# Optimization experiments

Measured on AMD Instinct MI355X. Metric: run time of the kernel, lower is better.

The kernel has to match this reference:

```python
import jax, jax.numpy as jnp
import numpy as np
from jax import lax

FT = 48   # feature map size (hardcoded as 48*48 in the torch decode)
C = 24    # backbone output channels
HC = 96   # head_conv
HEADS = {"hm_hp": 17, "hm": 1, "hps": 34, "hp_offset": 34}
DELTA = 1.8
SCALE = 0.02083333395421505  # ~1/48, exact literal from the module


def setup_inputs() -> dict:
    key = jax.random.key(0)
    ks = iter(jax.random.split(key, 64))
    inp = {"x": jax.random.normal(next(ks), (1, C, FT, FT), dtype=jnp.float32)}
    for h, cls in HEADS.items():
        inp[h + "_dw_w"] = jax.random.normal(next(ks), (C, 1, 3, 3), jnp.float32) * 0.1
        inp[h + "_dw_b"] = jax.random.normal(next(ks), (C,), jnp.float32) * 0.01
        inp[h + "_pw1_w"] = jax.random.normal(next(ks), (HC, C, 1, 1), jnp.float32) * 0.1
        inp[h + "_pw1_b"] = jax.random.normal(next(ks), (HC,), jnp.float32) * 0.01
        inp[h + "_pw2_w"] = jax.random.normal(next(ks), (cls, HC, 1, 1), jnp.float32) * 0.1
        inp[h + "_pw2_b"] = jax.random.normal(next(ks), (cls,), jnp.float32) * 0.01
    return inp


def _conv(x, w, groups=1):
    pad = "SAME" if w.shape[-1] == 3 else "VALID"
    return lax.conv_general_dilated(x, w, (1, 1), pad, feature_group_count=groups,
                                    dimension_numbers=("NCHW", "OIHW", "NCHW"))


def _head(x, dw_w, dw_b, pw1_w, pw1_b, pw2_w, pw2_b):
    y = _conv(x, dw_w, groups=C) + dw_b[None, :, None, None]
    y = jax.nn.relu(_conv(y, pw1_w) + pw1_b[None, :, None, None])
    return _conv(y, pw2_w) + pw2_b[None, :, None, None]


def _decode(hm_hp, hm, hps, hp_off):
    # NCHW [1,c,48,48] -> HWC
    kpt_heatmap = jax.nn.sigmoid(jnp.transpose(hm_hp[0], (1, 2, 0)))            # [48,48,17]
    center = jax.nn.sigmoid(jnp.transpose(hm[0], (1, 2, 0)))[:, :, 0]           # [48,48]
    kpt_regress = jnp.transpose(hps[0], (1, 2, 0)).reshape(FT * FT, 17, 2)
    kpt_offset = jnp.transpose(hp_off[0], (1, 2, 0)).reshape(FT * FT, 17, 2)

    rng = jnp.arange(FT, dtype=jnp.float32)
    gy = rng[:, None] - FT / 2.0
    gx = rng[None, :] - FT / 2.0
    w2c = 1.0 / (jnp.sqrt(gy * gy + gx * gx) + DELTA)                            # [48,48]

    # center-weighted argmax -> single center index
    ct = jnp.argmax((center * w2c).reshape(-1))
    ct_y = (ct // FT).astype(jnp.float32)
    ct_x = (ct % FT).astype(jnp.float32)

    kpt_coor = kpt_regress[ct] + jnp.stack([ct_y, ct_x])                         # [17,2]

    # distance-weighted per-keypoint argmax over the heatmap
    dy = rng[:, None, None] - kpt_coor[:, 0]                                     # [48,1,17]
    dx = rng[None, :, None] - kpt_coor[:, 1]                                     # [1,48,17]
    dist_weight = jnp.sqrt(dy * dy + dx * dx) + DELTA                            # [48,48,17]
    scores = (kpt_heatmap / dist_weight).reshape(FT * FT, 17)
    top = jnp.argmax(scores, axis=0)                                             # [17]

    ys = (top // FT).astype(jnp.float32)
    xs = (top % FT).astype(jnp.float32)
    k17 = jnp.arange(17)
    conf = kpt_heatmap.reshape(FT * FT, 17)[top, k17]                            # [17]
    off_yx = kpt_offset[top, k17]                                                # [17,2]
    coord = (off_yx + jnp.stack([ys, xs], axis=1)) * SCALE                       # [17,2]
    return jnp.concatenate([coord, conf[:, None]], axis=1).reshape(1, 1, 17, 3)


def _forward(x,
             hm_hp_dw_w, hm_hp_dw_b, hm_hp_pw1_w, hm_hp_pw1_b, hm_hp_pw2_w, hm_hp_pw2_b,
             hm_dw_w, hm_dw_b, hm_pw1_w, hm_pw1_b, hm_pw2_w, hm_pw2_b,
             hps_dw_w, hps_dw_b, hps_pw1_w, hps_pw1_b, hps_pw2_w, hps_pw2_b,
             hp_offset_dw_w, hp_offset_dw_b, hp_offset_pw1_w, hp_offset_pw1_b, hp_offset_pw2_w, hp_offset_pw2_b):
    x = x * 0.007843137718737125 - 1.0  # module's input normalization (backbone = identity)
    hm_hp = _head(x, hm_hp_dw_w, hm_hp_dw_b, hm_hp_pw1_w, hm_hp_pw1_b, hm_hp_pw2_w, hm_hp_pw2_b)
    hm = _head(x, hm_dw_w, hm_dw_b, hm_pw1_w, hm_pw1_b, hm_pw2_w, hm_pw2_b)
    hps = _head(x, hps_dw_w, hps_dw_b, hps_pw1_w, hps_pw1_b, hps_pw2_w, hps_pw2_b)
    hp_off = _head(x, hp_offset_dw_w, hp_offset_dw_b, hp_offset_pw1_w, hp_offset_pw1_b, hp_offset_pw2_w, hp_offset_pw2_b)
    return _decode(hm_hp, hm, hps, hp_off)


def reference(x,
              hm_hp_dw_w, hm_hp_dw_b, hm_hp_pw1_w, hm_hp_pw1_b, hm_hp_pw2_w, hm_hp_pw2_b,
              hm_dw_w, hm_dw_b, hm_pw1_w, hm_pw1_b, hm_pw2_w, hm_pw2_b,
              hps_dw_w, hps_dw_b, hps_pw1_w, hps_pw1_b, hps_pw2_w, hps_pw2_b,
              hp_offset_dw_w, hp_offset_dw_b, hp_offset_pw1_w, hp_offset_pw1_b, hp_offset_pw2_w, hp_offset_pw2_b):
    return _forward(x,
                    hm_hp_dw_w, hm_hp_dw_b, hm_hp_pw1_w, hm_hp_pw1_b, hm_hp_pw2_w, hm_hp_pw2_b,
                    hm_dw_w, hm_dw_b, hm_pw1_w, hm_pw1_b, hm_pw2_w, hm_pw2_b,
                    hps_dw_w, hps_dw_b, hps_pw1_w, hps_pw1_b, hps_pw2_w, hps_pw2_b,
                    hp_offset_dw_w, hp_offset_dw_b, hp_offset_pw1_w, hp_offset_pw1_b, hp_offset_pw2_w, hp_offset_pw2_b)
```

## Files before the change

kernel.cpp:

```cpp
#include <hip/hip_runtime.h>
#include <math.h>

#define FT 48
#define NPIX 2304
#define CIN 24
#define HC 96
#define NORM_SCALE 0.007843137718737125f
#define OUT_SCALE 0.02083333395421505f
#define DELTA 1.8f
#define NPROD 144
#define NDEC 17

__device__ int g_counter = 0;
__device__ int g_done = 0;

struct PF {
    const float* x;
    const float* w[4][6];
    float* hmhp_sig;
    float* pval;
    int*   pidx;
    float* out;
};

__device__ __forceinline__ float sigmoidf_(float v) { return 1.0f / (1.0f + expf(-v)); }

__global__ __launch_bounds__(256) void fused(PF p)
{
    __shared__ float s_dww[216];
    __shared__ float s_dwb[24];
    __shared__ float s_pw1w[HC * CIN];
    __shared__ float s_pw1b[HC];
    __shared__ float s_pw2t[HC * 17];
    __shared__ float s_pw2b[17];
    __shared__ float sv[4];
    __shared__ int si[4];
    __shared__ int s_ticket;
    __shared__ float s2_dww[2][216];
    __shared__ float s2_dwb[2][24];
    __shared__ float s2_pw1[2][HC * CIN];
    __shared__ float s2_pw1b[2][HC];
    __shared__ float s2_pw2[2][2 * HC];
    __shared__ float s2_pw2b[2][2];
    __shared__ float s_red[256];
    __shared__ int s_redi[256];
    __shared__ float s_dwv[CIN];
    __shared__ float sA[HC];
    __shared__ float s_ky, s_kx;
    __shared__ int s_ct, s_top;

    const int t = threadIdx.x;
    const int b = blockIdx.x;
    const bool is_hm = (b >= 72);
    const int lb = is_hm ? b - 72 : b;
    const int head = is_hm ? 1 : 0;

    const float* dw_w  = p.w[head][0];
    const float* dw_b  = p.w[head][1];
    const float* pw1_w = p.w[head][2];
    const float* pw1_b = p.w[head][3];
    const float* pw2_w = p.w[head][4];
    const float* pw2_b = p.w[head][5];

    if (t < 216) s_dww[t] = dw_w[t];
    if (t < 24) s_dwb[t] = dw_b[t];
    for (int i = t; i < HC * CIN; i += 256) s_pw1w[i] = pw1_w[i];
    if (t < HC) s_pw1b[t] = pw1_b[t];
    if (!is_hm) {
        for (int i = t; i < HC * 17; i += 256) {
            const int co = i / 17, k = i - co * 17;
            s_pw2t[i] = pw2_w[k * HC + co];
        }
        if (t < 17) s_pw2b[t] = pw2_b[t];
    } else {
        if (t < HC) s_pw2t[t] = pw2_w[t];
        if (t == 0) s_pw2b[0] = pw2_b[0];
    }

    const int lane = t & 63;
    const int split = lane & 7;
    const int pix = lb * 32 + (t >> 3);
    const int py = pix / FT;
    const int px = pix % FT;

    float xt[3][9];
#pragma unroll
    for (int c = 0; c < 3; ++c) {
        const int ci = split * 3 + c;
#pragma unroll
        for (int ky = 0; ky < 3; ++ky) {
            const int yy = py + ky - 1;
#pragma unroll
            for (int kx = 0; kx < 3; ++kx) {
                const int xx = px + kx - 1;
                float v = 0.0f;
                if (yy >= 0 && yy < FT && xx >= 0 && xx < FT)
                    v = p.x[ci * NPIX + yy * FT + xx] * NORM_SCALE - 1.0f;
                xt[c][ky * 3 + kx] = v;
            }
        }
    }
    __syncthreads();

    float part[3];
#pragma unroll
    for (int c = 0; c < 3; ++c) {
        const int ci = split * 3 + c;
        float acc = s_dwb[ci];
#pragma unroll
        for (int tap = 0; tap < 9; ++tap)
            acc = fmaf(s_dww[ci * 9 + tap], xt[c][tap], acc);
        part[c] = acc;
    }

    float dwv[CIN];
    const int gbase = lane & ~7;
#pragma unroll
    for (int ci = 0; ci < CIN; ++ci) {
        const float v = (ci % 3 == 0) ? part[0] : ((ci % 3 == 1) ? part[1] : part[2]);
        dwv[ci] = __shfl(v, gbase | (ci / 3), 64);
    }

    if (!is_hm) {
        float oacc[17];
#pragma unroll
        for (int k = 0; k < 17; ++k) oacc[k] = 0.0f;
#pragma unroll 4
        for (int j = 0; j < 12; ++j) {
            const int co = j * 8 + split;
            float a = s_pw1b[co];
#pragma unroll
            for (int ci = 0; ci < CIN; ++ci)
                a = fmaf(s_pw1w[co * CIN + ci], dwv[ci], a);
            a = fmaxf(a, 0.0f);
#pragma unroll
            for (int k = 0; k < 17; ++k)
                oacc[k] = fmaf(s_pw2t[co * 17 + k], a, oacc[k]);
        }
#pragma unroll
        for (int off = 1; off < 8; off <<= 1)
#pragma unroll
            for (int k = 0; k < 17; ++k)
                oacc[k] += __shfl_xor(oacc[k], off, 64);
        {
            int k = split;
            p.hmhp_sig[k * NPIX + pix] = sigmoidf_(oacc[k] + s_pw2b[k]);
            k = split + 8;
            p.hmhp_sig[k * NPIX + pix] = sigmoidf_(oacc[k] + s_pw2b[k]);
            if (split == 0)
                p.hmhp_sig[16 * NPIX + pix] = sigmoidf_(oacc[16] + s_pw2b[16]);
        }
    } else {
        float acc1 = 0.0f;
#pragma unroll 4
        for (int j = 0; j < 12; ++j) {
            const int co = j * 8 + split;
            float a = s_pw1b[co];
#pragma unroll
            for (int ci = 0; ci < CIN; ++ci)
                a = fmaf(s_pw1w[co * CIN + ci], dwv[ci], a);
            a = fmaxf(a, 0.0f);
            acc1 = fmaf(s_pw2t[co], a, acc1);
        }
#pragma unroll
        for (int off = 1; off < 8; off <<= 1)
            acc1 += __shfl_xor(acc1, off, 64);

        float v = -1e30f;
        int idx = pix;
        if (split == 0) {
            const float o = acc1 + s_pw2b[0];
            const float gy = (float)py - 24.0f, gx = (float)px - 24.0f;
            const float w = 1.0f / (sqrtf(gy * gy + gx * gx) + DELTA);
            v = sigmoidf_(o) * w;
        }
#pragma unroll
        for (int off = 1; off < 64; off <<= 1) {
            const float v2 = __shfl_xor(v, off, 64);
            const int i2 = __shfl_xor(idx, off, 64);
            if (v2 > v || (v2 == v && i2 < idx)) { v = v2; idx = i2; }
        }
        if (lane == 0) { sv[t >> 6] = v; si[t >> 6] = idx; }
        __syncthreads();
        if (t == 0) {
            float bv = sv[0]; int bi = si[0];
#pragma unroll
            for (int w2 = 1; w2 < 4; ++w2)
                if (sv[w2] > bv || (sv[w2] == bv && si[w2] < bi)) { bv = sv[w2]; bi = si[w2]; }
            p.pval[lb] = bv;
            p.pidx[lb] = bi;
        }
    }

    __syncthreads();
    if (t == 0) {
        __threadfence();
        s_ticket = atomicAdd(&g_counter, 1);
    }
    __syncthreads();
    const int ticket = s_ticket;
    if (ticket < NPROD - NDEC) return;
    const int k = ticket - (NPROD - NDEC);

    for (int i = t; i < HC * CIN; i += 256) {
        s2_pw1[0][i] = p.w[2][2][i];
        s2_pw1[1][i] = p.w[3][2][i];
    }
    if (t < HC) {
        s2_pw1b[0][t] = p.w[2][3][t];
        s2_pw1b[1][t] = p.w[3][3][t];
        s2_pw2[0][t]      = p.w[2][4][(2 * k) * HC + t];
        s2_pw2[0][HC + t] = p.w[2][4][(2 * k + 1) * HC + t];
        s2_pw2[1][t]      = p.w[3][4][(2 * k) * HC + t];
        s2_pw2[1][HC + t] = p.w[3][4][(2 * k + 1) * HC + t];
    }
    if (t < 216) { s2_dww[0][t] = p.w[2][0][t]; s2_dww[1][t] = p.w[3][0][t]; }
    if (t < 24)  { s2_dwb[0][t] = p.w[2][1][t]; s2_dwb[1][t] = p.w[3][1][t]; }
    if (t < 2)   { s2_pw2b[0][t] = p.w[2][5][2 * k + t]; s2_pw2b[1][t] = p.w[3][5][2 * k + t]; }

    if (t == 0) {
        while (__hip_atomic_load(&g_counter, __ATOMIC_ACQUIRE, __HIP_MEMORY_SCOPE_AGENT) < NPROD)
            __builtin_amdgcn_s_sleep(2);
    }
    __syncthreads();
    __threadfence();

    float r[9];
#pragma unroll
    for (int j = 0; j < 9; ++j)
        r[j] = p.hmhp_sig[k * NPIX + 256 * j + t];

    if (t < 64) {
        float v = p.pval[t];
        int i = p.pidx[t];
        if (t < 8) {
            const float v2 = p.pval[64 + t];
            const int i2 = p.pidx[64 + t];
            if (v2 > v || (v2 == v && i2 < i)) { v = v2; i = i2; }
        }
#pragma unroll
        for (int off = 1; off < 64; off <<= 1) {
            const float v2 = __shfl_xor(v, off, 64);
            const int i2 = __shfl_xor(i, off, 64);
            if (v2 > v || (v2 == v && i2 < i)) { v = v2; i = i2; }
        }
        if (t == 0) s_ct = i;
    }
    __syncthreads();
    const int ct = s_ct;
    const float cty = (float)(ct / FT);
    const float ctx = (float)(ct % FT);

    if (t < CIN) {
        const int cpy = ct / FT, cpx = ct % FT;
        float acc = s2_dwb[0][t];
#pragma unroll
        for (int ky = 0; ky < 3; ++ky) {
            const int yy = cpy + ky - 1;
#pragma unroll
            for (int kx = 0; kx < 3; ++kx) {
                const int xx = cpx + kx - 1;
                float v = 0.0f;
                if (yy >= 0 && yy < FT && xx >= 0 && xx < FT)
                    v = p.x[t * NPIX + yy * FT + xx] * NORM_SCALE - 1.0f;
                acc = fmaf(s2_dww[0][t * 9 + ky * 3 + kx], v, acc);
            }
        }
        s_dwv[t] = acc;
    }
    __syncthreads();
    if (t < HC) {
        float a = s2_pw1b[0][t];
#pragma unroll
        for (int ci = 0; ci < CIN; ++ci)
            a = fmaf(s2_pw1[0][t * CIN + ci], s_dwv[ci], a);
        sA[t] = fmaxf(a, 0.0f);
    }
    __syncthreads();
    if (t < 64) {
        float vy = 0.0f, vx = 0.0f;
        for (int co = t; co < HC; co += 64) {
            const float av = sA[co];
            vy = fmaf(s2_pw2[0][co], av, vy);
            vx = fmaf(s2_pw2[0][HC + co], av, vx);
        }
#pragma unroll
        for (int off = 1; off < 64; off <<= 1) {
            vy += __shfl_xor(vy, off, 64);
            vx += __shfl_xor(vx, off, 64);
        }
        if (t == 0) {
            s_ky = vy + s2_pw2b[0][0] + cty;
            s_kx = vx + s2_pw2b[0][1] + ctx;
        }
    }
    __syncthreads();
    const float kcy = s_ky, kcx = s_kx;

    float best = -1e30f;
    int bi = 0x7fffffff;
#pragma unroll
    for (int j = 0; j < 9; ++j) {
        const int i = 256 * j + t;
        const int y = i / FT, xx = i % FT;
        const float dy = (float)y - kcy, dx = (float)xx - kcx;
        const float d = sqrtf(dy * dy + dx * dx) + DELTA;
        const float v = r[j] / d;
        if (v > best || (v == best && i < bi)) { best = v; bi = i; }
    }
    s_red[t] = best;
    s_redi[t] = bi;
    __syncthreads();
    for (int s = 128; s > 0; s >>= 1) {
        if (t < s) {
            const float v2 = s_red[t + s];
            const int i2 = s_redi[t + s];
            if (v2 > s_red[t] || (v2 == s_red[t] && i2 < s_redi[t])) {
                s_red[t] = v2;
                s_redi[t] = i2;
            }
        }
        __syncthreads();
    }
    if (t == 0) s_top = s_redi[0];
    __syncthreads();
    const int top = s_top;

    if (t < CIN) {
        const int tpy = top / FT, tpx = top % FT;
        float acc = s2_dwb[1][t];
#pragma unroll
        for (int ky = 0; ky < 3; ++ky) {
            const int yy = tpy + ky - 1;
#pragma unroll
            for (int kx = 0; kx < 3; ++kx) {
                const int xx = tpx + kx - 1;
                float v = 0.0f;
                if (yy >= 0 && yy < FT && xx >= 0 && xx < FT)
                    v = p.x[t * NPIX + yy * FT + xx] * NORM_SCALE - 1.0f;
                acc = fmaf(s2_dww[1][t * 9 + ky * 3 + kx], v, acc);
            }
        }
        s_dwv[t] = acc;
    }
    __syncthreads();
    if (t < HC) {
        float a = s2_pw1b[1][t];
#pragma unroll
        for (int ci = 0; ci < CIN; ++ci)
            a = fmaf(s2_pw1[1][t * CIN + ci], s_dwv[ci], a);
        sA[t] = fmaxf(a, 0.0f);
    }
    __syncthreads();
    if (t < 64) {
        float oy = 0.0f, ox = 0.0f;
        for (int co = t; co < HC; co += 64) {
            const float av = sA[co];
            oy = fmaf(s2_pw2[1][co], av, oy);
            ox = fmaf(s2_pw2[1][HC + co], av, ox);
        }
#pragma unroll
        for (int off = 1; off < 64; off <<= 1) {
            oy += __shfl_xor(oy, off, 64);
            ox += __shfl_xor(ox, off, 64);
        }
        if (t == 0) {
            const float ty = (float)(top / FT), tx = (float)(top % FT);
            p.out[k * 3 + 0] = (oy + s2_pw2b[1][0] + ty) * OUT_SCALE;
            p.out[k * 3 + 1] = (ox + s2_pw2b[1][1] + tx) * OUT_SCALE;
            p.out[k * 3 + 2] = p.hmhp_sig[k * NPIX + top];
        }
    }

    __syncthreads();
    if (t == 0) {
        const int d = atomicAdd(&g_done, 1);
        if (d == NDEC - 1) {
            __hip_atomic_store(&g_done, 0, __ATOMIC_RELAXED, __HIP_MEMORY_SCOPE_AGENT);
            __hip_atomic_store(&g_counter, 0, __ATOMIC_RELEASE, __HIP_MEMORY_SCOPE_AGENT);
        }
    }
}


extern "C" void kernel_launch(void* const* d_in, const int* in_sizes, int n_in,
                              void* d_out, int out_size, void* d_ws, size_t ws_size,
                              hipStream_t stream)
{
    (void)in_sizes; (void)n_in; (void)out_size; (void)ws_size;

    float* ws = (float*)d_ws;
    float* hmhp_sig = ws;
    float* pval     = ws + 17 * NPIX;
    int*   pidx     = (int*)(ws + 17 * NPIX + 72);

    PF p;
    p.x = (const float*)d_in[0];
    for (int h = 0; h < 4; ++h)
        for (int j = 0; j < 6; ++j)
            p.w[h][j] = (const float*)d_in[1 + h * 6 + j];
    p.hmhp_sig = hmhp_sig;
    p.pval = pval;
    p.pidx = pidx;
    p.out = (float*)d_out;

    fused<<<NPROD, 256, 0, stream>>>(p);
}
```

Measured before the change: 132.3 us.

## Split fused kernel into heads and decode kernels, vectorize pointwise LDS reads

Replaces the single persistent kernel, which used an atomic ticket plus a spin-wait to let the last 17 blocks run the decode, with two ordinary launches on the same stream. The pointwise convolutions now read weights from LDS as float4, with the pw2 transpose padded to a stride of 20 so rows stay 16-byte aligned, and the channel loop is fully unrolled. The decode argmax switches from a shared-memory tree with many barriers to wave shuffles followed by a 4-way combine. This removes the global atomics and spin-wait but adds a second launch and the gap between kernels.

New measurement: 130.6 us. Within noise of the previous version (-1.3%).

```diff
diff --git a/kernel.cpp b/kernel.cpp
--- a/kernel.cpp
+++ b/kernel.cpp
@@ -8,59 +8,41 @@
 #define NORM_SCALE 0.007843137718737125f
 #define OUT_SCALE 0.02083333395421505f
 #define DELTA 1.8f
-#define NPROD 144
-#define NDEC 17
-
-__device__ int g_counter = 0;
-__device__ int g_done = 0;
-
-struct PF {
+
+__device__ __forceinline__ float sigmoidf_(float v) { return 1.0f / (1.0f + expf(-v)); }
+
+
+struct P1 {
     const float* x;
-    const float* w[4][6];
+    const float* hmhp_w[6];
+    const float* hm_w[6];
     float* hmhp_sig;
     float* pval;
     int*   pidx;
-    float* out;
 };
 
-__device__ __forceinline__ float sigmoidf_(float v) { return 1.0f / (1.0f + expf(-v)); }
-
-__global__ __launch_bounds__(256) void fused(PF p)
+__global__ __launch_bounds__(256) void k1_heads(P1 p)
 {
     __shared__ float s_dww[216];
     __shared__ float s_dwb[24];
     __shared__ float s_pw1w[HC * CIN];
     __shared__ float s_pw1b[HC];
-    __shared__ float s_pw2t[HC * 17];
+    __shared__ float s_pw2t[HC * 20];
     __shared__ float s_pw2b[17];
     __shared__ float sv[4];
     __shared__ int si[4];
-    __shared__ int s_ticket;
-    __shared__ float s2_dww[2][216];
-    __shared__ float s2_dwb[2][24];
-    __shared__ float s2_pw1[2][HC * CIN];
-    __shared__ float s2_pw1b[2][HC];
-    __shared__ float s2_pw2[2][2 * HC];
-    __shared__ float s2_pw2b[2][2];
-    __shared__ float s_red[256];
-    __shared__ int s_redi[256];
-    __shared__ float s_dwv[CIN];
-    __shared__ float sA[HC];
-    __shared__ float s_ky, s_kx;
-    __shared__ int s_ct, s_top;
 
     const int t = threadIdx.x;
     const int b = blockIdx.x;
     const bool is_hm = (b >= 72);
     const int lb = is_hm ? b - 72 : b;
-    const int head = is_hm ? 1 : 0;
-
-    const float* dw_w  = p.w[head][0];
-    const float* dw_b  = p.w[head][1];
-    const float* pw1_w = p.w[head][2];
-    const float* pw1_b = p.w[head][3];
-    const float* pw2_w = p.w[head][4];
-    const float* pw2_b = p.w[head][5];
+
+    const float* dw_w  = is_hm ? p.hm_w[0] : p.hmhp_w[0];
+    const float* dw_b  = is_hm ? p.hm_w[1] : p.hmhp_w[1];
+    const float* pw1_w = is_hm ? p.hm_w[2] : p.hmhp_w[2];
+    const float* pw1_b = is_hm ? p.hm_w[3] : p.hmhp_w[3];
+    const float* pw2_w = is_hm ? p.hm_w[4] : p.hmhp_w[4];
+    const float* pw2_b = is_hm ? p.hm_w[5] : p.hmhp_w[5];
 
     if (t < 216) s_dww[t] = dw_w[t];
     if (t < 24) s_dwb[t] = dw_b[t];
@@ -69,11 +51,11 @@
     if (!is_hm) {
         for (int i = t; i < HC * 17; i += 256) {
             const int co = i / 17, k = i - co * 17;
-            s_pw2t[i] = pw2_w[k * HC + co];
+            s_pw2t[co * 20 + k] = pw2_w[k * HC + co];
         }
         if (t < 17) s_pw2b[t] = pw2_b[t];
     } else {
-        if (t < HC) s_pw2t[t] = pw2_w[t];
+        if (t < HC) s_pw2t[t * 20] = pw2_w[t];
         if (t == 0) s_pw2b[0] = pw2_b[0];
     }
 
@@ -125,17 +107,30 @@
         float oacc[17];
 #pragma unroll
         for (int k = 0; k < 17; ++k) oacc[k] = 0.0f;
-#pragma unroll 4
+#pragma unroll
         for (int j = 0; j < 12; ++j) {
             const int co = j * 8 + split;
+            const float4* w4 = (const float4*)&s_pw1w[co * CIN];
             float a = s_pw1b[co];
 #pragma unroll
-            for (int ci = 0; ci < CIN; ++ci)
-                a = fmaf(s_pw1w[co * CIN + ci], dwv[ci], a);
+            for (int q = 0; q < 6; ++q) {
+                const float4 wv = w4[q];
+                a = fmaf(wv.x, dwv[4 * q + 0], a);
+                a = fmaf(wv.y, dwv[4 * q + 1], a);
+                a = fmaf(wv.z, dwv[4 * q + 2], a);
+                a = fmaf(wv.w, dwv[4 * q + 3], a);
+            }
             a = fmaxf(a, 0.0f);
-#pragma unroll
-            for (int k = 0; k < 17; ++k)
-                oacc[k] = fmaf(s_pw2t[co * 17 + k], a, oacc[k]);
+            const float4* q4 = (const float4*)&s_pw2t[co * 20];
+#pragma unroll
+            for (int q = 0; q < 4; ++q) {
+                const float4 qq = q4[q];
+                oacc[4 * q + 0] = fmaf(qq.x, a, oacc[4 * q + 0]);
+                oacc[4 * q + 1] = fmaf(qq.y, a, oacc[4 * q + 1]);
+                oacc[4 * q + 2] = fmaf(qq.z, a, oacc[4 * q + 2]);
+                oacc[4 * q + 3] = fmaf(qq.w, a, oacc[4 * q + 3]);
+            }
+            oacc[16] = fmaf(s_pw2t[co * 20 + 16], a, oacc[16]);
         }
 #pragma unroll
         for (int off = 1; off < 8; off <<= 1)
@@ -152,15 +147,21 @@
         }
     } else {
         float acc1 = 0.0f;
-#pragma unroll 4
+#pragma unroll
         for (int j = 0; j < 12; ++j) {
             const int co = j * 8 + split;
+            const float4* w4 = (const float4*)&s_pw1w[co * CIN];
             float a = s_pw1b[co];
 #pragma unroll
-            for (int ci = 0; ci < CIN; ++ci)
-                a = fmaf(s_pw1w[co * CIN + ci], dwv[ci], a);
+            for (int q = 0; q < 6; ++q) {
+                const float4 wv = w4[q];
+                a = fmaf(wv.x, dwv[4 * q + 0], a);
+                a = fmaf(wv.y, dwv[4 * q + 1], a);
+                a = fmaf(wv.z, dwv[4 * q + 2], a);
+                a = fmaf(wv.w, dwv[4 * q + 3], a);
+            }
             a = fmaxf(a, 0.0f);
-            acc1 = fmaf(s_pw2t[co], a, acc1);
+            acc1 = fmaf(s_pw2t[co * 20], a, acc1);
         }
 #pragma unroll
         for (int off = 1; off < 8; off <<= 1)
@@ -191,44 +192,58 @@
             p.pidx[lb] = bi;
         }
     }
-
-    __syncthreads();
-    if (t == 0) {
-        __threadfence();
-        s_ticket = atomicAdd(&g_counter, 1);
-    }
-    __syncthreads();
-    const int ticket = s_ticket;
-    if (ticket < NPROD - NDEC) return;
-    const int k = ticket - (NPROD - NDEC);
-
-    for (int i = t; i < HC * CIN; i += 256) {
-        s2_pw1[0][i] = p.w[2][2][i];
-        s2_pw1[1][i] = p.w[3][2][i];
-    }
-    if (t < HC) {
-        s2_pw1b[0][t] = p.w[2][3][t];
-        s2_pw1b[1][t] = p.w[3][3][t];
-        s2_pw2[0][t]      = p.w[2][4][(2 * k) * HC + t];
-        s2_pw2[0][HC + t] = p.w[2][4][(2 * k + 1) * HC + t];
-        s2_pw2[1][t]      = p.w[3][4][(2 * k) * HC + t];
-        s2_pw2[1][HC + t] = p.w[3][4][(2 * k + 1) * HC + t];
-    }
-    if (t < 216) { s2_dww[0][t] = p.w[2][0][t]; s2_dww[1][t] = p.w[3][0][t]; }
-    if (t < 24)  { s2_dwb[0][t] = p.w[2][1][t]; s2_dwb[1][t] = p.w[3][1][t]; }
-    if (t < 2)   { s2_pw2b[0][t] = p.w[2][5][2 * k + t]; s2_pw2b[1][t] = p.w[3][5][2 * k + t]; }
-
-    if (t == 0) {
-        while (__hip_atomic_load(&g_counter, __ATOMIC_ACQUIRE, __HIP_MEMORY_SCOPE_AGENT) < NPROD)
-            __builtin_amdgcn_s_sleep(2);
-    }
-    __syncthreads();
-    __threadfence();
+}
+
+
+struct P2 {
+    const float* x;
+    const float* hps_w[6];
+    const float* hpo_w[6];
+    const float* hmhp_sig;
+    const float* pval;
+    const int*   pidx;
+    float* out;
+};
+
+__global__ __launch_bounds__(256) void k2_decode(P2 p)
+{
+    __shared__ float s2_dww[2][216];
+    __shared__ float s2_dwb[2][24];
+    __shared__ float s2_pw1[2][HC * CIN];
+    __shared__ float s2_pw1b[2][HC];
+    __shared__ float s2_pw2[2][2 * HC];
+    __shared__ float s2_pw2b[2][2];
+    __shared__ float s_red[4];
+    __shared__ int s_redi[4];
+    __shared__ float s_dwv[CIN];
+    __shared__ float sA[HC];
+    __shared__ float s_ky, s_kx;
+    __shared__ int s_ct, s_top;
+
+    const int t = threadIdx.x;
+    const int k = blockIdx.x;
+    const int lane = t & 63;
+    const int wv = t >> 6;
 
     float r[9];
 #pragma unroll
     for (int j = 0; j < 9; ++j)
         r[j] = p.hmhp_sig[k * NPIX + 256 * j + t];
+    for (int i = t; i < HC * CIN; i += 256) {
+        s2_pw1[0][i] = p.hps_w[2][i];
+        s2_pw1[1][i] = p.hpo_w[2][i];
+    }
+    if (t < HC) {
+        s2_pw1b[0][t] = p.hps_w[3][t];
+        s2_pw1b[1][t] = p.hpo_w[3][t];
+        s2_pw2[0][t]      = p.hps_w[4][(2 * k) * HC + t];
+        s2_pw2[0][HC + t] = p.hps_w[4][(2 * k + 1) * HC + t];
+        s2_pw2[1][t]      = p.hpo_w[4][(2 * k) * HC + t];
+        s2_pw2[1][HC + t] = p.hpo_w[4][(2 * k + 1) * HC + t];
+    }
+    if (t < 216) { s2_dww[0][t] = p.hps_w[0][t]; s2_dww[1][t] = p.hpo_w[0][t]; }
+    if (t < 24)  { s2_dwb[0][t] = p.hps_w[1][t]; s2_dwb[1][t] = p.hpo_w[1][t]; }
+    if (t < 2)   { s2_pw2b[0][t] = p.hps_w[5][2 * k + t]; s2_pw2b[1][t] = p.hpo_w[5][2 * k + t]; }
 
     if (t < 64) {
         float v = p.pval[t];
@@ -308,21 +323,21 @@
         const float v = r[j] / d;
         if (v > best || (v == best && i < bi)) { best = v; bi = i; }
     }
-    s_red[t] = best;
-    s_redi[t] = bi;
-    __syncthreads();
-    for (int s = 128; s > 0; s >>= 1) {
-        if (t < s) {
-            const float v2 = s_red[t + s];
-            const int i2 = s_redi[t + s];
-            if (v2 > s_red[t] || (v2 == s_red[t] && i2 < s_redi[t])) {
-                s_red[t] = v2;
-                s_redi[t] = i2;
-            }
-        }
-        __syncthreads();
-    }
-    if (t == 0) s_top = s_redi[0];
+#pragma unroll
+    for (int off = 1; off < 64; off <<= 1) {
+        const float v2 = __shfl_xor(best, off, 64);
+        const int i2 = __shfl_xor(bi, off, 64);
+        if (v2 > best || (v2 == best && i2 < bi)) { best = v2; bi = i2; }
+    }
+    if (lane == 0) { s_red[wv] = best; s_redi[wv] = bi; }
+    __syncthreads();
+    if (t == 0) {
+        float bv = s_red[0]; int bb = s_redi[0];
+#pragma unroll
+        for (int w2 = 1; w2 < 4; ++w2)
+            if (s_red[w2] > bv || (s_red[w2] == bv && s_redi[w2] < bb)) { bv = s_red[w2]; bb = s_redi[w2]; }
+        s_top = bb;
+    }
     __syncthreads();
     const int top = s_top;
 
@@ -371,15 +386,6 @@
             p.out[k * 3 + 2] = p.hmhp_sig[k * NPIX + top];
         }
     }
-
-    __syncthreads();
-    if (t == 0) {
-        const int d = atomicAdd(&g_done, 1);
-        if (d == NDEC - 1) {
-            __hip_atomic_store(&g_done, 0, __ATOMIC_RELAXED, __HIP_MEMORY_SCOPE_AGENT);
-            __hip_atomic_store(&g_counter, 0, __ATOMIC_RELEASE, __HIP_MEMORY_SCOPE_AGENT);
-        }
-    }
 }
 
 
@@ -394,15 +400,23 @@
     float* pval     = ws + 17 * NPIX;
     int*   pidx     = (int*)(ws + 17 * NPIX + 72);
 
-    PF p;
-    p.x = (const float*)d_in[0];
-    for (int h = 0; h < 4; ++h)
-        for (int j = 0; j < 6; ++j)
-            p.w[h][j] = (const float*)d_in[1 + h * 6 + j];
-    p.hmhp_sig = hmhp_sig;
-    p.pval = pval;
-    p.pidx = pidx;
-    p.out = (float*)d_out;
-
-    fused<<<NPROD, 256, 0, stream>>>(p);
+    P1 p1;
+    p1.x = (const float*)d_in[0];
+    for (int j = 0; j < 6; ++j) p1.hmhp_w[j] = (const float*)d_in[1 + j];
+    for (int j = 0; j < 6; ++j) p1.hm_w[j]   = (const float*)d_in[7 + j];
+    p1.hmhp_sig = hmhp_sig;
+    p1.pval = pval;
+    p1.pidx = pidx;
+
+    P2 p2;
+    p2.x = (const float*)d_in[0];
+    for (int j = 0; j < 6; ++j) p2.hps_w[j] = (const float*)d_in[13 + j];
+    for (int j = 0; j < 6; ++j) p2.hpo_w[j] = (const float*)d_in[19 + j];
+    p2.hmhp_sig = hmhp_sig;
+    p2.pval = pval;
+    p2.pidx = pidx;
+    p2.out = (float*)d_out;
+
+    k1_heads<<<144, 256, 0, stream>>>(p1);
+    k2_decode<<<17, 256, 0, stream>>>(p2);
 }
```
